# Kernel optimization log

Measured on AMD Instinct MI355X. Metric: run time of the kernel, lower is better.

The kernel has to match this reference:

```python
import jax, jax.numpy as jnp
import numpy as np

B, HW, N_L = 8, 5476, 32
DIM, L_IN, KC, VC, NH = 1024, 768, 1024, 1024, 8
EPS = 1e-5


def conv1(w, b, x):
    # 1x1 Conv1d == per-position linear. x: [B, C_in, L] -> [B, C_out, L]
    return jnp.einsum('oc,bcl->bol', w, x) + b[None, :, None]


def inorm(y):
    # InstanceNorm1d (affine=False): normalize each (batch, channel) over length.
    m = jnp.mean(y, axis=-1, keepdims=True)
    v = jnp.var(y, axis=-1, keepdims=True)
    return (y - m) * jax.lax.rsqrt(v + EPS)


def setup_inputs() -> dict:
    key = jax.random.key(0)
    ks = jax.random.split(key, 10)
    s = 0.02  # weight init scale
    x = jax.random.normal(ks[0], (B, HW, DIM), jnp.float32)
    l = jax.random.normal(ks[1], (B, N_L, L_IN), jnp.float32)
    l_mask = jax.random.randint(ks[2], (B, N_L, 1), 0, 2).astype(jnp.float32)
    l_mask = l_mask.at[:, 0, :].set(1.0)  # ensure at least one valid token
    return {
        'x': x, 'l': l, 'l_mask': l_mask,
        'vis_w': jax.random.normal(ks[3], (DIM, DIM), jnp.float32) * s,
        'vis_b': jnp.zeros((DIM,), jnp.float32),
        'fq_w': jax.random.normal(ks[4], (KC, DIM), jnp.float32) * s,
        'fq_b': jnp.zeros((KC,), jnp.float32),
        'fk_w': jax.random.normal(ks[5], (KC, L_IN), jnp.float32) * s,
        'fk_b': jnp.zeros((KC,), jnp.float32),
        'fv_w': jax.random.normal(ks[6], (VC, L_IN), jnp.float32) * s,
        'fv_b': jnp.zeros((VC,), jnp.float32),
        'W_w': jax.random.normal(ks[7], (VC, VC), jnp.float32) * s,
        'W_b': jnp.zeros((VC,), jnp.float32),
        'pm_w': jax.random.normal(ks[8], (VC, VC), jnp.float32) * s,
        'pm_b': jnp.zeros((VC,), jnp.float32),
    }


def reference(x, l, l_mask, vis_w, vis_b, fq_w, fq_b, fk_w, fk_b,
              fv_w, fv_b, W_w, W_b, pm_w, pm_b):
    # PWAM forward (eval mode, dropout=0)
    b, hw, _ = x.shape
    n_l = l.shape[1]
    xt = jnp.transpose(x, (0, 2, 1))            # [B, dim, HW]
    lt = jnp.transpose(l, (0, 2, 1))            # [B, l_in, N_l]
    mt = jnp.transpose(l_mask, (0, 2, 1))       # [B, 1, N_l]

    # vis_project: conv1d + GELU
    vis = jax.nn.gelu(conv1(vis_w, vis_b, xt), approximate=False)  # [B, dim, HW]

    # SpatialImageLanguageAttention
    q = inorm(conv1(fq_w, fq_b, xt))            # [B, KC, HW]
    k = conv1(fk_w, fk_b, lt) * mt              # [B, KC, N_l]
    v = conv1(fv_w, fv_b, lt) * mt              # [B, VC, N_l]

    qh = q.reshape(b, NH, KC // NH, hw).transpose(0, 1, 3, 2)  # [B, H, HW, dk]
    kh = k.reshape(b, NH, KC // NH, n_l)                       # [B, H, dk, N_l]
    vh = v.reshape(b, NH, VC // NH, n_l)                       # [B, H, dv, N_l]

    sim = jnp.einsum('bhqd,bhdk->bhqk', qh, kh) * (KC ** -0.5)
    sim = sim + (10000.0 * mt[:, None] - 10000.0)              # masked bias
    sim = jax.nn.softmax(sim, axis=-1)                          # [B, H, HW, N_l]

    out = jnp.einsum('bhqk,bhdk->bhqd', sim, vh)                # [B, H, HW, dv]
    out = out.transpose(0, 2, 1, 3).reshape(b, hw, VC)          # [B, HW, VC]
    out = jnp.transpose(out, (0, 2, 1))                         # [B, VC, HW]
    lang = inorm(conv1(W_w, W_b, out))                          # [B, VC, HW]

    # gated fusion + project_mm
    mm = vis * lang
    mm = jax.nn.gelu(conv1(pm_w, pm_b, mm), approximate=False)
    return jnp.transpose(mm, (0, 2, 1))                         # [B, HW, VC]
```

## Files before the change

### kernel.cpp

```cpp
#include <hip/hip_runtime.h>

typedef _Float16 f16;
typedef _Float16 f16x4 __attribute__((ext_vector_type(4)));
typedef _Float16 f16x8 __attribute__((ext_vector_type(8)));
typedef float f32x4 __attribute__((ext_vector_type(4)));

#define NB   8
#define HW   5476
#define NL   32
#define DIM  1024
#define LIN  768
#define MTOT (NB * HW)
#define MT256 ((MTOT + 255) / 256)
#define CSPLIT 128


__device__ __forceinline__ void g2l16(const void* g, void* l) {
#if __has_builtin(__builtin_amdgcn_global_load_lds)
  __builtin_amdgcn_global_load_lds(
      (const __attribute__((address_space(1))) void*)g,
      (__attribute__((address_space(3))) void*)l, 16, 0, 0);
#else
  const int lane = threadIdx.x & 63;
  *(uint4*)((char*)l + lane * 16) = *(const uint4*)g;
#endif
}

__device__ __forceinline__ float gelu_f(float x) {
  return 0.5f * x * (1.0f + erff(x * 0.70710678118654752f));
}

#define WAITV(N) asm volatile("s_waitcnt vmcnt(" #N ")" ::: "memory")
__device__ __forceinline__ void barrier_nf() {
  asm volatile("s_barrier" ::: "memory");
}

__device__ __forceinline__ int swz32(int r, int q) {
  const int p = r >> 1;
  const int c = (((r & 1) << 2) | q) ^ (p & 7);
  return p * 64 + c * 8;
}

template <int EPI, int EPI2>
__global__ __launch_bounds__(512, 2) void gemm256(
    const f16* __restrict__ A, const f16* __restrict__ W,
    const float* __restrict__ bias, void* __restrict__ out,
    const f16* __restrict__ W2, const float* __restrict__ bias2,
    void* __restrict__ out2, int M) {
  constexpr int K = 1024, N = 1024;
  constexpr int KT = K / 32;
  constexpr int NT = (EPI2 >= 0) ? 8 : 4;
  constexpr int NWG = NT * MT256;
  constexpr int CHUNK = NWG / 8;
  __shared__ f16 lds[4][2][256 * 32];

  const int L = blockIdx.x;
  const int w = (L & 7) * CHUNK + (L >> 3);
  const int mt = w / NT;
  int nt = w % NT;
  const f16* Wp = W;
  const float* bp = bias;
  void* op = out;
  bool second = false;
  if constexpr (EPI2 >= 0) {
    if (nt >= 4) {
      nt -= 4;
      Wp = W2;
      bp = bias2;
      op = out2;
      second = true;
    }
  }

  const int tid = threadIdx.x;
  const int wave = tid >> 6, lane = tid & 63;
  const int m0 = mt * 256, n0 = nt * 256;
  const int wm = (wave >> 2) * 128;
  const int wn = (wave & 3) * 64;
  const int fr = lane & 15, fq = lane >> 4;

  f32x4 acc[8][4];
#pragma unroll
  for (int i = 0; i < 8; ++i)
#pragma unroll
    for (int j = 0; j < 4; ++j) acc[i][j] = (f32x4){0.f, 0.f, 0.f, 0.f};

  const int plocal = lane >> 3;
  const int csw = (lane & 7) ^ plocal;
  const int rofs = plocal * 2 + (csw >> 2);
  const int qofs = (csw & 3) * 8;

  auto stage = [&](int t) {
    const int buf = t & 3;
    const int k0 = t * 32;
    f16* Ab = &lds[buf][0][0];
    f16* Bb = &lds[buf][1][0];
#pragma unroll
    for (int la = 0; la < 2; ++la) {
      const int rg = wave * 2 + la;
      int gm = m0 + rg * 16 + rofs;
      if (gm > M - 1) gm = M - 1;
      g2l16(A + (size_t)gm * K + k0 + qofs, &Ab[rg * 512]);
    }
#pragma unroll
    for (int la = 0; la < 2; ++la) {
      const int rg = wave * 2 + la;
      const int gn = n0 + rg * 16 + rofs;
      g2l16(Wp + (size_t)gn * K + k0 + qofs, &Bb[rg * 512]);
    }
  };

  auto compute = [&](int t) {
    const f16* Ab = &lds[t & 3][0][0];
    const f16* Bb = &lds[t & 3][1][0];
    f16x8 af[8], bf[4];
#pragma unroll
    for (int i = 0; i < 8; ++i)
      af[i] = *(const f16x8*)&Ab[swz32(wm + i * 16 + fr, fq)];
#pragma unroll
    for (int j = 0; j < 4; ++j)
      bf[j] = *(const f16x8*)&Bb[swz32(wn + j * 16 + fr, fq)];
    __builtin_amdgcn_s_setprio(1);
#pragma unroll
    for (int i = 0; i < 8; ++i)
#pragma unroll
      for (int j = 0; j < 4; ++j)
        acc[i][j] = __builtin_amdgcn_mfma_f32_16x16x32_f16(af[i], bf[j],
                                                           acc[i][j], 0, 0, 0);
    __builtin_amdgcn_s_setprio(0);
  };

  stage(0);
  stage(1);
  stage(2);
#pragma unroll 4
  for (int t = 0; t < KT - 4; ++t) {
    WAITV(8);
    barrier_nf();
    stage(t + 3);
    compute(t);
  }
  WAITV(8); barrier_nf(); stage(KT - 1); compute(KT - 4);
  WAITV(8); barrier_nf(); compute(KT - 3);
  WAITV(4); barrier_nf(); compute(KT - 2);
  WAITV(0); barrier_nf(); compute(KT - 1);

  const bool do_gelu = second ? (EPI2 == 0 || EPI2 == 3) : (EPI == 0 || EPI == 3);
  const bool to_f16 = second ? (EPI2 <= 1) : (EPI <= 1);
  const int row0 = m0 + wm + fq * 4;
  const int col0 = n0 + wn + fr;
#pragma unroll
  for (int j = 0; j < 4; ++j) {
    const int col = col0 + j * 16;
    const float bv = bp[col];
#pragma unroll
    for (int i = 0; i < 8; ++i) {
#pragma unroll
      for (int r = 0; r < 4; ++r) {
        const int row = row0 + i * 16 + r;
        if (row < M) {
          float v = acc[i][j][r] + bv;
          if (do_gelu) v = gelu_f(v);
          if (to_f16)
            ((f16*)op)[(size_t)row * N + col] = (f16)v;
          else
            ((float*)op)[(size_t)row * N + col] = v;
        }
      }
    }
  }
}

__global__ void cvt_f32_f16(const float* __restrict__ in, f16* __restrict__ out,
                            int nchunks) {
  const int i = blockIdx.x * 256 + threadIdx.x;
  if (i >= nchunks) return;
  const float4* p = (const float4*)in + (size_t)i * 2;
  const float4 a = p[0], b = p[1];
  f16x8 o = {(f16)a.x, (f16)a.y, (f16)a.z, (f16)a.w,
             (f16)b.x, (f16)b.y, (f16)b.z, (f16)b.w};
  *((f16x8*)out + i) = o;
}

template <typename T>
__global__ __launch_bounds__(256) void colstats_partial(
    const T* __restrict__ X, float* __restrict__ psum,
    float* __restrict__ psq) {
  const int b = blockIdx.y;
  const int sp = blockIdx.x;
  const int c = threadIdx.x * 4;
  constexpr int CHUNK = (HW + CSPLIT - 1) / CSPLIT;
  const int r0 = sp * CHUNK;
  const int r1 = (r0 + CHUNK < HW) ? r0 + CHUNK : HW;

  float s0 = 0.f, s1 = 0.f, s2 = 0.f, s3 = 0.f;
  float q0 = 0.f, q1 = 0.f, q2 = 0.f, q3 = 0.f;
  const T* base = X + ((size_t)b * HW + r0) * DIM + c;
  for (int r = r0; r < r1; ++r) {
    float v0, v1, v2, v3;
    if constexpr (sizeof(T) == 2) {
      const f16x4 v = *(const f16x4*)base;
      v0 = (float)v[0]; v1 = (float)v[1]; v2 = (float)v[2]; v3 = (float)v[3];
    } else {
      const float4 v = *(const float4*)base;
      v0 = v.x; v1 = v.y; v2 = v.z; v3 = v.w;
    }
    s0 += v0; s1 += v1; s2 += v2; s3 += v3;
    q0 += v0 * v0; q1 += v1 * v1; q2 += v2 * v2; q3 += v3 * v3;
    base += DIM;
  }
  const size_t o = ((size_t)sp * NB + b) * DIM + c;
  *(float4*)&psum[o] = make_float4(s0, s1, s2, s3);
  *(float4*)&psq[o] = make_float4(q0, q1, q2, q3);
}

__global__ __launch_bounds__(256) void colstats_final(
    const float* __restrict__ psum, const float* __restrict__ psq,
    float* __restrict__ mean, float* __restrict__ rinv) {
  const int i = blockIdx.x * 256 + threadIdx.x;
  float s = 0.f, q = 0.f;
  for (int sp = 0; sp < CSPLIT; ++sp) {
    s += psum[(size_t)sp * NB * DIM + i];
    q += psq[(size_t)sp * NB * DIM + i];
  }
  const float m = s * (1.0f / HW);
  const float var = q * (1.0f / HW) - m * m;
  mean[i] = m;
  rinv[i] = rsqrtf(var + 1e-5f);
}

__global__ __launch_bounds__(256) void kv_gemm(
    const float* __restrict__ l, const float* __restrict__ lmask,
    const float* __restrict__ wk, const float* __restrict__ bk,
    const float* __restrict__ wv, const float* __restrict__ bv,
    float* __restrict__ Kout, float* __restrict__ Vout) {
  const int b = blockIdx.z;
  const int o0 = blockIdx.x * 64;
  const float* w = blockIdx.y ? wv : wk;
  const float* bb = blockIdx.y ? bv : bk;
  float* out = blockIdx.y ? Vout : Kout;

  __shared__ float wl[64 * 129];
  __shared__ float ll[32 * 129];
  const int tid = threadIdx.x;
  const int o = tid & 63, ng = tid >> 6;
  float acc[8];
#pragma unroll
  for (int j = 0; j < 8; ++j) acc[j] = 0.f;

  for (int kc = 0; kc < LIN; kc += 128) {
    for (int e = tid; e < 64 * 128; e += 256)
      wl[(e >> 7) * 129 + (e & 127)] =
          w[(size_t)(o0 + (e >> 7)) * LIN + kc + (e & 127)];
    for (int e = tid; e < 32 * 128; e += 256)
      ll[(e >> 7) * 129 + (e & 127)] =
          l[(size_t)b * NL * LIN + (size_t)(e >> 7) * LIN + kc + (e & 127)];
    __syncthreads();
    for (int k = 0; k < 128; ++k) {
      const float wv_ = wl[o * 129 + k];
#pragma unroll
      for (int j = 0; j < 8; ++j) acc[j] += wv_ * ll[(ng * 8 + j) * 129 + k];
    }
    __syncthreads();
  }
  const float bval = bb[o0 + o];
#pragma unroll
  for (int j = 0; j < 8; ++j) {
    const int n = ng * 8 + j;
    out[((size_t)b * DIM + o0 + o) * NL + n] =
        (acc[j] + bval) * lmask[b * NL + n];
  }
}

__global__ __launch_bounds__(256) void attn_kernel(
    const f16* __restrict__ Q, const float* __restrict__ qmean,
    const float* __restrict__ qrinv, const float* __restrict__ Kk,
    const float* __restrict__ Vv, const float* __restrict__ lmask,
    float* __restrict__ Out) {
  const int b = blockIdx.z, h = blockIdx.y;
  __shared__ float ks[128 * NL], vs[128 * NL], qm[128], qr[128], bs[NL];
  const int tid = threadIdx.x;
  const float* kbase = Kk + ((size_t)b * DIM + h * 128) * NL;
  const float* vbase = Vv + ((size_t)b * DIM + h * 128) * NL;
  for (int i = tid; i < 128 * NL; i += 256) {
    ks[i] = kbase[i];
    vs[i] = vbase[i];
  }
  if (tid < 128) {
    qm[tid] = qmean[b * DIM + h * 128 + tid];
    qr[tid] = qrinv[b * DIM + h * 128 + tid];
  }
  if (tid < NL) bs[tid] = (lmask[b * NL + tid] - 1.0f) * 10000.0f;
  __syncthreads();

  const int mloc = blockIdx.x * 256 + tid;
  if (mloc >= HW) return;
  const size_t m = (size_t)b * HW + mloc;
  const f16* qrow = Q + m * DIM + h * 128;

  float sc[32];
#pragma unroll
  for (int n = 0; n < 32; ++n) sc[n] = 0.f;

  for (int d8 = 0; d8 < 16; ++d8) {
    const f16x8 qv = *(const f16x8*)(qrow + d8 * 8);
#pragma unroll
    for (int j = 0; j < 8; ++j) {
      const int d = d8 * 8 + j;
      const float qd = ((float)qv[j] - qm[d]) * qr[d];
      const float4* kr = (const float4*)&ks[d * 32];
#pragma unroll
      for (int n4 = 0; n4 < 8; ++n4) {
        const float4 kk = kr[n4];
        sc[n4 * 4 + 0] += qd * kk.x;
        sc[n4 * 4 + 1] += qd * kk.y;
        sc[n4 * 4 + 2] += qd * kk.z;
        sc[n4 * 4 + 3] += qd * kk.w;
      }
    }
  }
  float mx = -1e30f;
#pragma unroll
  for (int n = 0; n < 32; ++n) {
    sc[n] = sc[n] * 0.03125f + bs[n];
    mx = fmaxf(mx, sc[n]);
  }
  float sum = 0.f;
#pragma unroll
  for (int n = 0; n < 32; ++n) {
    sc[n] = __expf(sc[n] - mx);
    sum += sc[n];
  }
  const float rs = 1.0f / sum;

  float* orow = Out + m * DIM + h * 128;
  for (int dv8 = 0; dv8 < 16; ++dv8) {
    float ov[8];
#pragma unroll
    for (int j = 0; j < 8; ++j) {
      const float4* vr = (const float4*)&vs[(dv8 * 8 + j) * 32];
      float a = 0.f;
#pragma unroll
      for (int n4 = 0; n4 < 8; ++n4) {
        const float4 vv = vr[n4];
        a += sc[n4 * 4 + 0] * vv.x + sc[n4 * 4 + 1] * vv.y +
             sc[n4 * 4 + 2] * vv.z + sc[n4 * 4 + 3] * vv.w;
      }
      ov[j] = a * rs;
    }
    float4* op = (float4*)(orow + dv8 * 8);
    op[0] = make_float4(ov[0], ov[1], ov[2], ov[3]);
    op[1] = make_float4(ov[4], ov[5], ov[6], ov[7]);
  }
}

__global__ void center_kernel(const float* __restrict__ X,
                              const float* __restrict__ mean,
                              f16* __restrict__ out, int nchunks) {
  const int i = blockIdx.x * 256 + threadIdx.x;
  if (i >= nchunks) return;
  const size_t e = (size_t)i * 8;
  const int mrow = (int)(e >> 10);
  const int o = (int)(e & 1023);
  const int b = mrow / HW;
  const float4* p = (const float4*)(X + e);
  const float4 a = p[0], c = p[1];
  const float* mn = mean + b * DIM + o;
  f16x8 r = {(f16)(a.x - mn[0]), (f16)(a.y - mn[1]), (f16)(a.z - mn[2]),
             (f16)(a.w - mn[3]), (f16)(c.x - mn[4]), (f16)(c.y - mn[5]),
             (f16)(c.z - mn[6]), (f16)(c.w - mn[7])};
  *((f16x8*)out + i) = r;
}

__global__ void fuse_kernel(const f16* __restrict__ vis,
                            const float* __restrict__ lang,
                            const float* __restrict__ mean,
                            const float* __restrict__ rinv,
                            f16* __restrict__ out, int nchunks) {
  const int i = blockIdx.x * 256 + threadIdx.x;
  if (i >= nchunks) return;
  const size_t e = (size_t)i * 8;
  const int mrow = (int)(e >> 10);
  const int o = (int)(e & 1023);
  const int b = mrow / HW;
  const f16x8 v = *((const f16x8*)vis + i);
  const float4* p = (const float4*)(lang + e);
  const float4 a = p[0], c = p[1];
  const float lv[8] = {a.x, a.y, a.z, a.w, c.x, c.y, c.z, c.w};
  const float* mn = mean + b * DIM + o;
  const float* ri = rinv + b * DIM + o;
  f16x8 r;
#pragma unroll
  for (int j = 0; j < 8; ++j)
    r[j] = (f16)((float)v[j] * ((lv[j] - mn[j]) * ri[j]));
  *((f16x8*)out + i) = r;
}

extern "C" void kernel_launch(void* const* d_in, const int* in_sizes, int n_in,
                              void* d_out, int out_size, void* d_ws,
                              size_t ws_size, hipStream_t stream) {
  const float* x     = (const float*)d_in[0];
  const float* l     = (const float*)d_in[1];
  const float* lmask = (const float*)d_in[2];
  const float* vis_w = (const float*)d_in[3];
  const float* vis_b = (const float*)d_in[4];
  const float* fq_w  = (const float*)d_in[5];
  const float* fq_b  = (const float*)d_in[6];
  const float* fk_w  = (const float*)d_in[7];
  const float* fk_b  = (const float*)d_in[8];
  const float* fv_w  = (const float*)d_in[9];
  const float* fv_b  = (const float*)d_in[10];
  const float* W_w   = (const float*)d_in[11];
  const float* W_b   = (const float*)d_in[12];
  const float* pm_w  = (const float*)d_in[13];
  const float* pm_b  = (const float*)d_in[14];

  char* ws = (char*)d_ws;
  const size_t SB = (size_t)MTOT * DIM * 2;
  f16* Ah = (f16*)(ws);
  f16* Bh = (f16*)(ws + SB);
  f16* Ch = (f16*)(ws + 2 * SB);
  float* Df = (float*)(ws + 3 * SB);
  char* wsp = ws + 5 * SB;
  f16* vis_wh = (f16*)(wsp);
  f16* fq_wh  = (f16*)(wsp + (1 << 21));
  f16* W_wh   = (f16*)(wsp + 2 * (1 << 21));
  f16* pm_wh  = (f16*)(wsp + 3 * (1 << 21));
  float* Kout = (float*)(wsp + 4 * (1 << 21));
  float* Vout = (float*)(wsp + 4 * (1 << 21) + (1 << 20));
  float* st   = (float*)(wsp + 4 * (1 << 21) + 2 * (1 << 20));
  float* qmean = st;
  float* qrinv = st + 8192;
  float* amean = st + 16384;
  float* arinv = st + 24576;
  float* lmean = st + 32768;
  float* lrinv = st + 40960;
  float* psum  = (float*)(wsp + 4 * (1 << 21) + 3 * (1 << 20));
  float* psq   = psum + (size_t)CSPLIT * NB * DIM;

  const int NCH_BIG = MTOT * DIM / 8;
  const int NCH_W = DIM * DIM / 8;

  cvt_f32_f16<<<(NCH_BIG + 255) / 256, 256, 0, stream>>>(x, Ah, NCH_BIG);
  cvt_f32_f16<<<(NCH_W + 255) / 256, 256, 0, stream>>>(vis_w, vis_wh, NCH_W);
  cvt_f32_f16<<<(NCH_W + 255) / 256, 256, 0, stream>>>(fq_w, fq_wh, NCH_W);
  cvt_f32_f16<<<(NCH_W + 255) / 256, 256, 0, stream>>>(W_w, W_wh, NCH_W);
  cvt_f32_f16<<<(NCH_W + 255) / 256, 256, 0, stream>>>(pm_w, pm_wh, NCH_W);

  kv_gemm<<<dim3(16, 2, 8), 256, 0, stream>>>(l, lmask, fk_w, fk_b, fv_w, fv_b,
                                              Kout, Vout);

  gemm256<0, 1><<<8 * MT256, 512, 0, stream>>>(
      Ah, vis_wh, vis_b, Bh, fq_wh, fq_b, Ch, MTOT);

  colstats_partial<f16><<<dim3(CSPLIT, NB), 256, 0, stream>>>(Ch, psum, psq);
  colstats_final<<<32, 256, 0, stream>>>(psum, psq, qmean, qrinv);

  attn_kernel<<<dim3((HW + 255) / 256, 8, 8), 256, 0, stream>>>(
      Ch, qmean, qrinv, Kout, Vout, lmask, Df);

  colstats_partial<float><<<dim3(CSPLIT, NB), 256, 0, stream>>>(Df, psum, psq);
  colstats_final<<<32, 256, 0, stream>>>(psum, psq, amean, arinv);
  center_kernel<<<(NCH_BIG + 255) / 256, 256, 0, stream>>>(Df, amean, Ah,
                                                           NCH_BIG);

  gemm256<2, -1><<<4 * MT256, 512, 0, stream>>>(
      Ah, W_wh, W_b, Df, nullptr, nullptr, nullptr, MTOT);
  colstats_partial<float><<<dim3(CSPLIT, NB), 256, 0, stream>>>(Df, psum, psq);
  colstats_final<<<32, 256, 0, stream>>>(psum, psq, lmean, lrinv);
  fuse_kernel<<<(NCH_BIG + 255) / 256, 256, 0, stream>>>(Bh, Df, lmean, lrinv,
                                                         Ah, NCH_BIG);

  gemm256<3, -1><<<4 * MT256, 512, 0, stream>>>(
      Ah, pm_wh, pm_b, d_out, nullptr, nullptr, nullptr, MTOT);
}
```

Baseline: 1.439 ms.

## Fuse attention-output column mean into attention kernel and reorder GEMM tiles

The attention kernel now reduces its output per column with wave shuffles and atomically accumulates per-block partial sums, replacing a separate full pass of column statistics over the fp32 attention output; only the mean is finalized since centering needs just that. GEMM workgroup mapping switches to iterate M tiles fastest within each N tile, changing cache reuse pattern, and the epilogue hoists bias loads and reorders loops. Adds a memset and atomics, and out-of-range threads now do redundant compute.

```diff
diff --git a/kernel.cpp b/kernel.cpp
--- a/kernel.cpp
+++ b/kernel.cpp
@@ -13,6 +13,7 @@
 #define MTOT (NB * HW)
 #define MT256 ((MTOT + 255) / 256)
 #define CSPLIT 128
+#define ASPLIT 22
 
 
 __device__ __forceinline__ void g2l16(const void* g, void* l) {
@@ -56,8 +57,8 @@
 
   const int L = blockIdx.x;
   const int w = (L & 7) * CHUNK + (L >> 3);
-  const int mt = w / NT;
-  int nt = w % NT;
+  const int mt = w % MT256;
+  int nt = w / MT256;
   const f16* Wp = W;
   const float* bp = bias;
   void* op = out;
@@ -149,22 +150,23 @@
   const bool to_f16 = second ? (EPI2 <= 1) : (EPI <= 1);
   const int row0 = m0 + wm + fq * 4;
   const int col0 = n0 + wn + fr;
-#pragma unroll
-  for (int j = 0; j < 4; ++j) {
-    const int col = col0 + j * 16;
-    const float bv = bp[col];
-#pragma unroll
-    for (int i = 0; i < 8; ++i) {
-#pragma unroll
-      for (int r = 0; r < 4; ++r) {
-        const int row = row0 + i * 16 + r;
-        if (row < M) {
-          float v = acc[i][j][r] + bv;
+  float bv[4];
+#pragma unroll
+  for (int j = 0; j < 4; ++j) bv[j] = bp[col0 + j * 16];
+#pragma unroll
+  for (int i = 0; i < 8; ++i) {
+#pragma unroll
+    for (int r = 0; r < 4; ++r) {
+      const int row = row0 + i * 16 + r;
+      if (row < M) {
+#pragma unroll
+        for (int j = 0; j < 4; ++j) {
+          float v = acc[i][j][r] + bv[j];
           if (do_gelu) v = gelu_f(v);
           if (to_f16)
-            ((f16*)op)[(size_t)row * N + col] = (f16)v;
+            ((f16*)op)[(size_t)row * N + col0 + j * 16] = (f16)v;
           else
-            ((float*)op)[(size_t)row * N + col] = v;
+            ((float*)op)[(size_t)row * N + col0 + j * 16] = v;
         }
       }
     }
@@ -229,6 +231,14 @@
   rinv[i] = rsqrtf(var + 1e-5f);
 }
 
+__global__ __launch_bounds__(256) void asum_final(
+    const float* __restrict__ psum, float* __restrict__ mean) {
+  const int i = blockIdx.x * 256 + threadIdx.x;
+  float s = 0.f;
+  for (int sp = 0; sp < ASPLIT; ++sp) s += psum[(size_t)sp * NB * DIM + i];
+  mean[i] = s * (1.0f / HW);
+}
+
 __global__ __launch_bounds__(256) void kv_gemm(
     const float* __restrict__ l, const float* __restrict__ lmask,
     const float* __restrict__ wk, const float* __restrict__ bk,
@@ -276,7 +286,7 @@
     const f16* __restrict__ Q, const float* __restrict__ qmean,
     const float* __restrict__ qrinv, const float* __restrict__ Kk,
     const float* __restrict__ Vv, const float* __restrict__ lmask,
-    float* __restrict__ Out) {
+    float* __restrict__ Out, float* __restrict__ psum) {
   const int b = blockIdx.z, h = blockIdx.y;
   __shared__ float ks[128 * NL], vs[128 * NL], qm[128], qr[128], bs[NL];
   const int tid = threadIdx.x;
@@ -294,8 +304,9 @@
   __syncthreads();
 
   const int mloc = blockIdx.x * 256 + tid;
-  if (mloc >= HW) return;
-  const size_t m = (size_t)b * HW + mloc;
+  const bool valid = mloc < HW;
+  const int mc = valid ? mloc : HW - 1;
+  const size_t m = (size_t)b * HW + mc;
   const f16* qrow = Q + m * DIM + h * 128;
 
   float sc[32];
@@ -334,6 +345,7 @@
   const float rs = 1.0f / sum;
 
   float* orow = Out + m * DIM + h * 128;
+  float* pbase = psum + ((size_t)blockIdx.x * NB + b) * DIM + h * 128;
   for (int dv8 = 0; dv8 < 16; ++dv8) {
     float ov[8];
 #pragma unroll
@@ -348,9 +360,22 @@
       }
       ov[j] = a * rs;
     }
-    float4* op = (float4*)(orow + dv8 * 8);
-    op[0] = make_float4(ov[0], ov[1], ov[2], ov[3]);
-    op[1] = make_float4(ov[4], ov[5], ov[6], ov[7]);
+    if (valid) {
+      float4* op = (float4*)(orow + dv8 * 8);
+      op[0] = make_float4(ov[0], ov[1], ov[2], ov[3]);
+      op[1] = make_float4(ov[4], ov[5], ov[6], ov[7]);
+    }
+#pragma unroll
+    for (int j = 0; j < 8; ++j) {
+      float v = valid ? ov[j] : 0.f;
+      v += __shfl_down(v, 32);
+      v += __shfl_down(v, 16);
+      v += __shfl_down(v, 8);
+      v += __shfl_down(v, 4);
+      v += __shfl_down(v, 2);
+      v += __shfl_down(v, 1);
+      if ((tid & 63) == 0) atomicAdd(&pbase[dv8 * 8 + j], v);
+    }
   }
 }
 
@@ -456,11 +481,10 @@
   colstats_partial<f16><<<dim3(CSPLIT, NB), 256, 0, stream>>>(Ch, psum, psq);
   colstats_final<<<32, 256, 0, stream>>>(psum, psq, qmean, qrinv);
 
+  hipMemsetAsync(psum, 0, (size_t)ASPLIT * NB * DIM * sizeof(float), stream);
   attn_kernel<<<dim3((HW + 255) / 256, 8, 8), 256, 0, stream>>>(
-      Ch, qmean, qrinv, Kout, Vout, lmask, Df);
-
-  colstats_partial<float><<<dim3(CSPLIT, NB), 256, 0, stream>>>(Df, psum, psq);
-  colstats_final<<<32, 256, 0, stream>>>(psum, psq, amean, arinv);
+      Ch, qmean, qrinv, Kout, Vout, lmask, Df, psum);
+  asum_final<<<32, 256, 0, stream>>>(psum, amean);
   center_kernel<<<(NCH_BIG + 255) / 256, 256, 0, stream>>>(Df, amean, Ah,
                                                            NCH_BIG);
 
```

New measurement: 1.474 ms. 1.02x slower.
